# Performance work log

Hardware: AMD Instinct MI355X
Metric: run time of the kernel (lower is better)

Reference implementation:

```python
import jax, jax.numpy as jnp
import numpy as np

N_OSC = 2  # n: oscillator group size (pairwise oscillators)


def group_norm(c, w, b, num_groups, eps=1e-5):
    # c: [B, C, N]; torch.nn.GroupNorm semantics over (group-channels, N)
    B, C, N = c.shape
    g = c.reshape(B, num_groups, C // num_groups, N)
    mu = g.mean(axis=(2, 3), keepdims=True)
    var = g.var(axis=(2, 3), keepdims=True)
    g = (g - mu) / jnp.sqrt(var + eps)
    return g.reshape(B, C, N) * w[None, :, None] + b[None, :, None]


def normalize(x, n=N_OSC, eps=1e-6):
    # project each size-n group of channels onto the unit sphere
    B, N, C = x.shape
    v = x.reshape(B, N, C // n, n)
    nrm = jnp.linalg.norm(v, axis=-1, keepdims=True)
    return (v / (nrm + eps)).reshape(B, N, C)


def setup_inputs():
    key = jax.random.key(0)
    ks = jax.random.split(key, 4)
    B, C, N = 2, 16, 8192
    x = jax.random.normal(ks[0], (B, C, N), jnp.float32)
    c = jax.random.normal(ks[1], (B, C, N), jnp.float32)
    sc = jax.random.uniform(ks[2], (1, N, N), jnp.float32)  # dense structural connectivity
    gn_w = jnp.ones((C,), jnp.float32)
    gn_b = jnp.zeros((C,), jnp.float32)
    # learned per-edge coupling weight; scaled ~1/N so coupling is O(1)
    conn_w = jax.random.normal(ks[3], (N, N), jnp.float32) * (1.0 / N)
    # OmegaLayer param: init_omg * (1/sqrt(2)) * ones((ch//2, 1))
    omg_param = jnp.full((C // 2, 1), 1.0 / np.sqrt(2), jnp.float32)
    gamma = jnp.ones((1,), jnp.float32)
    return {"x": x, "c": c, "sc": sc, "gn_w": gn_w, "gn_b": gn_b,
            "conn_w": conn_w, "omg_param": omg_param, "gamma": gamma, "Q": 8}


def reference(x, c, sc, gn_w, gn_b, conn_w, omg_param, gamma, Q):
    n = N_OSC
    C = x.shape[1]
    # c_norm (GroupNorm with ch//n groups) then transpose [B,C,N] -> [B,N,C]
    y = group_norm(c, gn_w, gn_b, C // n)
    y = jnp.swapaxes(y, 1, 2)  # [B,N,C]
    xt = jnp.swapaxes(x, 1, 2)  # [B,N,C]
    A = sc[0] * conn_w  # weighted adjacency [N,N]
    omg = jnp.abs(omg_param)[None, None, :, 0]  # [1,1,C//2]; norm over last dim == abs
    g = gamma.reshape(())
    xt = normalize(xt)
    B, N, _ = xt.shape

    def step(xk, _):
        coup = jnp.einsum('mn,bnc->bmc', A, xk)  # graph coupling
        yt = coup + y
        xv = xk.reshape(B, N, C // n, n)
        yv = yt.reshape(B, N, C // n, n)
        sim = jnp.sum(xv * yv, axis=-1, keepdims=True)  # <x, y> per group
        y_proj = (yv - sim * xv).reshape(B, N, C)  # tangent projection
        xp = xk.reshape(B, N, C // 2, 2)
        omg_x = jnp.stack([omg * xp[..., 1], -omg * xp[..., 0]], axis=-1).reshape(B, N, C)
        xn = normalize(xk + g * (omg_x + y_proj))
        return xn, xn

    _, xs = jax.lax.scan(step, xt, None, length=Q)
    return xs  # [Q, B, N, C] (stacked list of per-step states)
```

## Files before the change

### kernel.cpp

```cpp
#include <hip/hip_runtime.h>
#include <hip/hip_bf16.h>

#define NB 2
#define NC 16
#define NN 8192
#define NBC 32
#define KS 16
#define SROWS 16
#define SWAVES 8
#define STEP_ELEMS (NB * NN * NC)

typedef float f32x4 __attribute__((ext_vector_type(4)));
typedef __bf16 bf16x8 __attribute__((ext_vector_type(8)));

__global__ void gn_stats_k(const float* __restrict__ c, float* __restrict__ stats) {
    int bg = blockIdx.x;
    const float* p = c + (size_t)bg * 16384;
    float s = 0.f, ss = 0.f;
    for (int i = threadIdx.x; i < 4096; i += 256) {
        float4 v = ((const float4*)p)[i];
        s  += v.x + v.y + v.z + v.w;
        ss += v.x*v.x + v.y*v.y + v.z*v.z + v.w*v.w;
    }
    #pragma unroll
    for (int o = 32; o; o >>= 1) { s += __shfl_down(s, o); ss += __shfl_down(ss, o); }
    __shared__ float sh[8];
    int w = threadIdx.x >> 6;
    if ((threadIdx.x & 63) == 0) { sh[w] = s; sh[w + 4] = ss; }
    __syncthreads();
    if (threadIdx.x == 0) {
        float S = sh[0]+sh[1]+sh[2]+sh[3], SS = sh[4]+sh[5]+sh[6]+sh[7];
        float mu = S * (1.f/16384.f);
        float var = SS * (1.f/16384.f) - mu*mu;
        stats[bg*2]   = mu;
        stats[bg*2+1] = rsqrtf(var + 1e-5f);
    }
}

__global__ void prep_xy_k(const float* __restrict__ x, const float* __restrict__ c,
                          const float* __restrict__ gnw, const float* __restrict__ gnb,
                          const float* __restrict__ stats,
                          float* __restrict__ y_arr, float* __restrict__ x0f,
                          __bf16* __restrict__ Xbf) {
    int tid = blockIdx.x * 256 + threadIdx.x;
    int n = tid & (NN - 1);
    int j = (tid >> 13) & 7;
    int b = tid >> 16;
    int ch0 = 2 * j;
    size_t r0 = ((size_t)(b * NC + ch0)) * NN + n;
    float c0 = c[r0], c1 = c[r0 + NN];
    float x0 = x[r0], x1 = x[r0 + NN];
    float mu = stats[(b*8 + j)*2], rstd = stats[(b*8 + j)*2 + 1];
    float y0 = (c0 - mu) * rstd * gnw[ch0]   + gnb[ch0];
    float y1 = (c1 - mu) * rstd * gnw[ch0+1] + gnb[ch0+1];
    int base = n * NBC + b * NC + ch0;
    y_arr[base] = y0; y_arr[base + 1] = y1;
    float inv = 1.f / (sqrtf(x0*x0 + x1*x1) + 1e-6f);
    x0 *= inv; x1 *= inv;
    size_t xi = ((size_t)(b * NN + n)) * NC + ch0;
    x0f[xi] = x0; x0f[xi + 1] = x1;
    Xbf[(size_t)(b*NC + ch0)     * NN + n] = (__bf16)x0;
    Xbf[(size_t)(b*NC + ch0 + 1) * NN + n] = (__bf16)x1;
}

__device__ inline bf16x8 cvt8(f32x4 s0, f32x4 s1, f32x4 w0, f32x4 w1) {
    bf16x8 r;
    r[0]=(__bf16)(s0[0]*w0[0]); r[1]=(__bf16)(s0[1]*w0[1]);
    r[2]=(__bf16)(s0[2]*w0[2]); r[3]=(__bf16)(s0[3]*w0[3]);
    r[4]=(__bf16)(s1[0]*w1[0]); r[5]=(__bf16)(s1[1]*w1[1]);
    r[6]=(__bf16)(s1[2]*w1[2]); r[7]=(__bf16)(s1[3]*w1[3]);
    return r;
}

__global__ __launch_bounds__(256) void prep_A_frag_k(const float* __restrict__ sc,
                                                     const float* __restrict__ cw,
                                                     __bf16* __restrict__ Af) {
    __shared__ __align__(16) __bf16 tb[16][520];
    int t = threadIdx.x;
    int p  = blockIdx.x >> 4;
    int kc = blockIdx.x & 15;
    #pragma unroll
    for (int it = 0; it < 4; ++it) {
        int e = it * 2048 + t * 8;
        int row = e >> 9;
        int kloc = e & 511;
        size_t src = (size_t)(p * 16 + row) * NN + kc * 512 + kloc;
        f32x4 s0 = ((const f32x4*)(sc + src))[0], s1 = ((const f32x4*)(sc + src))[1];
        f32x4 w0 = ((const f32x4*)(cw + src))[0], w1 = ((const f32x4*)(cw + src))[1];
        bf16x8 o = cvt8(s0, s1, w0, w1);
        int k32 = kloc >> 5;
        int lane_f = row + (((kloc & 31) >> 3) << 4);
        *(bf16x8*)(&tb[k32][lane_f * 8]) = o;
    }
    __syncthreads();
    size_t obase = ((size_t)p * 256 + kc * 16) * 512;
    #pragma unroll
    for (int it = 0; it < 4; ++it) {
        int f = it * 256 + t;
        int k32 = f >> 6;
        int lf  = f & 63;
        bf16x8 v = *(const bf16x8*)(&tb[k32][lf * 8]);
        *(bf16x8*)(Af + obase + (size_t)f * 8) = v;
    }
}

__global__ __launch_bounds__(512, 4) void gemm_frag_k(
    const __bf16* __restrict__ Af, const __bf16* __restrict__ Xc,
    float* __restrict__ coup)
{
    __shared__ float red[SWAVES][SROWS][36];
    int tid = threadIdx.x;
    int lane = tid & 63, w = tid >> 6;
    int mb = blockIdx.x;

    const __bf16* ap = Af + ((size_t)mb * 256 + w * 32) * 512 + lane * 8;
    int fr = lane & 15;
    int kg = (lane >> 4) * 8;
    const __bf16* xb0 = Xc + (size_t)fr * NN + w * 1024 + kg;
    const __bf16* xb1 = xb0 + (size_t)16 * NN;

    f32x4 acc0 = {0.f,0.f,0.f,0.f}, acc1 = {0.f,0.f,0.f,0.f};

    bf16x8 a0  = *(const bf16x8*)(ap);
    bf16x8 a1  = *(const bf16x8*)(ap + 512);
    bf16x8 b00 = *(const bf16x8*)(xb0);
    bf16x8 b01 = *(const bf16x8*)(xb0 + 32);
    bf16x8 b10 = *(const bf16x8*)(xb1);
    bf16x8 b11 = *(const bf16x8*)(xb1 + 32);
    #pragma unroll
    for (int it = 0; it < 15; ++it) {
        bf16x8 na0  = *(const bf16x8*)(ap  + (2 * it + 2) * 512);
        bf16x8 na1  = *(const bf16x8*)(ap  + (2 * it + 3) * 512);
        bf16x8 nb00 = *(const bf16x8*)(xb0 + it * 64 + 64);
        bf16x8 nb01 = *(const bf16x8*)(xb0 + it * 64 + 96);
        bf16x8 nb10 = *(const bf16x8*)(xb1 + it * 64 + 64);
        bf16x8 nb11 = *(const bf16x8*)(xb1 + it * 64 + 96);
        acc0 = __builtin_amdgcn_mfma_f32_16x16x32_bf16(a0, b00, acc0, 0, 0, 0);
        acc1 = __builtin_amdgcn_mfma_f32_16x16x32_bf16(a0, b10, acc1, 0, 0, 0);
        acc0 = __builtin_amdgcn_mfma_f32_16x16x32_bf16(a1, b01, acc0, 0, 0, 0);
        acc1 = __builtin_amdgcn_mfma_f32_16x16x32_bf16(a1, b11, acc1, 0, 0, 0);
        a0 = na0; a1 = na1; b00 = nb00; b01 = nb01; b10 = nb10; b11 = nb11;
    }
    acc0 = __builtin_amdgcn_mfma_f32_16x16x32_bf16(a0, b00, acc0, 0, 0, 0);
    acc1 = __builtin_amdgcn_mfma_f32_16x16x32_bf16(a0, b10, acc1, 0, 0, 0);
    acc0 = __builtin_amdgcn_mfma_f32_16x16x32_bf16(a1, b01, acc0, 0, 0, 0);
    acc1 = __builtin_amdgcn_mfma_f32_16x16x32_bf16(a1, b11, acc1, 0, 0, 0);

    int orow = (lane >> 4) * 4, ocol = lane & 15;
    #pragma unroll
    for (int r4 = 0; r4 < 4; ++r4) {
        red[w][orow + r4][ocol]      = acc0[r4];
        red[w][orow + r4][ocol + 16] = acc1[r4];
    }
    __syncthreads();

    if (tid < SROWS * 16) {
        int ch2 = tid & 15;
        int r_  = tid >> 4;
        float c0 = 0.f, c1 = 0.f;
        #pragma unroll
        for (int ww = 0; ww < SWAVES; ++ww) {
            c0 += red[ww][r_][2 * ch2];
            c1 += red[ww][r_][2 * ch2 + 1];
        }
        int n_ = mb * SROWS + r_;
        coup[(size_t)n_ * NBC + 2 * ch2]     = c0;
        coup[(size_t)n_ * NBC + 2 * ch2 + 1] = c1;
    }
}

__global__ void update_coup_k(const float* __restrict__ coup, const float* __restrict__ y_arr,
                              const float* __restrict__ omg, const float* __restrict__ gamma,
                              float* __restrict__ x0f, __bf16* __restrict__ Xbf,
                              float* __restrict__ out_k) {
    int tid = blockIdx.x * 256 + threadIdx.x;
    int pi = tid & 15;
    int b = pi >> 3, j = pi & 7;
    int n = tid >> 4;
    int base = n * NBC + b * NC + 2 * j;
    float c0 = coup[base];
    float c1 = coup[base + 1];
    float y0 = y_arr[base] + c0;
    float y1 = y_arr[base + 1] + c1;
    size_t xi = ((size_t)(b * NN + n)) * NC + 2 * j;
    float x0 = x0f[xi], x1 = x0f[xi + 1];
    float sim = x0 * y0 + x1 * y1;
    float p0 = y0 - sim * x0;
    float p1 = y1 - sim * x1;
    float om = fabsf(omg[j]);
    float g  = gamma[0];
    float v0 = x0 + g * ( om * x1 + p0);
    float v1 = x1 + g * (-om * x0 + p1);
    float inv = 1.f / (sqrtf(v0*v0 + v1*v1) + 1e-6f);
    v0 *= inv; v1 *= inv;
    out_k[xi] = v0; out_k[xi + 1] = v1;
    x0f[xi] = v0; x0f[xi + 1] = v1;
    Xbf[(size_t)(b*NC + 2*j)     * NN + n] = (__bf16)v0;
    Xbf[(size_t)(b*NC + 2*j + 1) * NN + n] = (__bf16)v1;
}

__device__ inline bf16x8 mulcvt8(const float* __restrict__ s, const float* __restrict__ w) {
    f32x4 s0 = ((const f32x4*)s)[0], s1 = ((const f32x4*)s)[1];
    f32x4 w0 = ((const f32x4*)w)[0], w1 = ((const f32x4*)w)[1];
    return cvt8(s0, s1, w0, w1);
}

__global__ __launch_bounds__(256) void gemm_step_fused_k(const float* __restrict__ sc,
                                                         const float* __restrict__ cw,
                                                         const __bf16* __restrict__ Xbf,
                                                         float* __restrict__ part) {
    int mb = blockIdx.x;
    int ks = blockIdx.y;
    int lane = threadIdx.x & 63;
    int w = threadIdx.x >> 6;
    int row = mb * 64 + w * 16 + (lane & 15);
    int kb  = (lane >> 4) * 8;
    int k0  = ks * (NN / KS);
    const int KC = NN / KS;
    f32x4 acc0 = {0.f,0.f,0.f,0.f}, acc1 = {0.f,0.f,0.f,0.f};
    const __bf16* bp0 = Xbf + (size_t)(lane & 15) * NN + k0 + kb;
    const __bf16* bp1 = bp0 + (size_t)16 * NN;
    const float* as = sc + (size_t)row * NN + k0 + kb;
    const float* aw = cw + (size_t)row * NN + k0 + kb;
    #pragma unroll 4
    for (int k = 0; k < KC; k += 32) {
        bf16x8 a  = mulcvt8(as + k, aw + k);
        bf16x8 b0 = *(const bf16x8*)(bp0 + k);
        bf16x8 b1 = *(const bf16x8*)(bp1 + k);
        acc0 = __builtin_amdgcn_mfma_f32_16x16x32_bf16(a, b0, acc0, 0, 0, 0);
        acc1 = __builtin_amdgcn_mfma_f32_16x16x32_bf16(a, b1, acc1, 0, 0, 0);
    }
    int orow = mb * 64 + w * 16 + (lane >> 4) * 4;
    int ocol = lane & 15;
    float* pp = part + (size_t)ks * NN * NBC + (size_t)orow * NBC + ocol;
    #pragma unroll
    for (int r = 0; r < 4; ++r) {
        pp[(size_t)r * NBC]      = acc0[r];
        pp[(size_t)r * NBC + 16] = acc1[r];
    }
}

__global__ void update_step_k(const float* __restrict__ part, const float* __restrict__ y_arr,
                              const float* __restrict__ omg, const float* __restrict__ gamma,
                              float* __restrict__ x0f, __bf16* __restrict__ Xbf,
                              float* __restrict__ out_k) {
    int tid = blockIdx.x * 256 + threadIdx.x;
    int pi = tid & 15;
    int b = pi >> 3, j = pi & 7;
    int n = tid >> 4;
    int base = n * NBC + b * NC + 2 * j;
    float c0 = 0.f, c1 = 0.f;
    #pragma unroll
    for (int ks = 0; ks < KS; ++ks) {
        const float* p = part + (size_t)ks * NN * NBC + base;
        c0 += p[0]; c1 += p[1];
    }
    float y0 = y_arr[base] + c0;
    float y1 = y_arr[base + 1] + c1;
    size_t xi = ((size_t)(b * NN + n)) * NC + 2 * j;
    float x0 = x0f[xi], x1 = x0f[xi + 1];
    float sim = x0 * y0 + x1 * y1;
    float p0 = y0 - sim * x0;
    float p1 = y1 - sim * x1;
    float om = fabsf(omg[j]);
    float g  = gamma[0];
    float v0 = x0 + g * ( om * x1 + p0);
    float v1 = x1 + g * (-om * x0 + p1);
    float inv = 1.f / (sqrtf(v0*v0 + v1*v1) + 1e-6f);
    v0 *= inv; v1 *= inv;
    out_k[xi] = v0; out_k[xi + 1] = v1;
    x0f[xi] = v0; x0f[xi + 1] = v1;
    Xbf[(size_t)(b*NC + 2*j)     * NN + n] = (__bf16)v0;
    Xbf[(size_t)(b*NC + 2*j + 1) * NN + n] = (__bf16)v1;
}

extern "C" void kernel_launch(void* const* d_in, const int* in_sizes, int n_in,
                              void* d_out, int out_size, void* d_ws, size_t ws_size,
                              hipStream_t stream) {
    const float* x     = (const float*)d_in[0];
    const float* c     = (const float*)d_in[1];
    const float* sc    = (const float*)d_in[2];
    const float* gnw   = (const float*)d_in[3];
    const float* gnb   = (const float*)d_in[4];
    const float* cw    = (const float*)d_in[5];
    const float* omg   = (const float*)d_in[6];
    const float* gamma = (const float*)d_in[7];
    float* out = (float*)d_out;
    int Q = out_size / STEP_ELEMS;

    const size_t szA    = (size_t)NN * NN * 2;
    const size_t szX    = (size_t)NBC * NN * 2;
    const size_t szX0f  = (size_t)NB * NN * NC * 4;
    const size_t szY    = (size_t)NN * NBC * 4;
    const size_t szCoup = (size_t)NN * NBC * 4;
    const size_t szPart = (size_t)KS * NN * NBC * 4;
    const size_t rest = szX + szX0f + szY + szCoup + szPart + 256;
    bool bigws = ws_size >= szA + rest;

    char* p = (char*)d_ws;
    __bf16* Af = nullptr;
    if (bigws) { Af = (__bf16*)p; p += szA; }
    __bf16* Xbf  = (__bf16*)p; p += szX;
    float* x0f   = (float*)p;  p += szX0f;
    float* y_arr = (float*)p;  p += szY;
    float* coup  = (float*)p;  p += szCoup;
    float* part  = (float*)p;  p += szPart;
    float* stats = (float*)p;  p += 256;

    gn_stats_k<<<16, 256, 0, stream>>>(c, stats);
    prep_xy_k<<<(NB * NN * 8) / 256, 256, 0, stream>>>(x, c, gnw, gnb, stats, y_arr, x0f, Xbf);

    if (bigws) {
        prep_A_frag_k<<<(NN / 16) * (NN / 512), 256, 0, stream>>>(sc, cw, Af);
        for (int q = 0; q < Q; ++q) {
            gemm_frag_k<<<NN / SROWS, SWAVES * 64, 0, stream>>>(Af, Xbf, coup);
            update_coup_k<<<(NB * NN * 8) / 256, 256, 0, stream>>>(
                coup, y_arr, omg, gamma, x0f, Xbf, out + (size_t)q * STEP_ELEMS);
        }
    } else {
        dim3 gg(NN / 64, KS);
        for (int q = 0; q < Q; ++q) {
            gemm_step_fused_k<<<gg, 256, 0, stream>>>(sc, cw, Xbf, part);
            update_step_k<<<(NB * NN * 8) / 256, 256, 0, stream>>>(
                part, y_arr, omg, gamma, x0f, Xbf, out + (size_t)q * STEP_ELEMS);
        }
    }
}
```

Before: 459.8 us.

## Process two row-blocks per GEMM workgroup with 16 waves and pad prep LDS

The per-step GEMM workgroup now computes 32 output rows instead of 16. It uses 16 waves, each covering a 512-wide K slice, so every loaded X fragment feeds MFMAs for two A row-blocks. This halves the grid and aims to cut redundant X loads from memory. The A-fragment prep kernel changes its LDS tile layout to a padded [16][4][17][8] shape, presumably to avoid bank conflicts, and issues its loads two at a time. The 1024-thread blocks with a larger reduction buffer may lower occupancy and lengthen the cross-wave reduction.

```diff
diff --git a/kernel.cpp b/kernel.cpp
--- a/kernel.cpp
+++ b/kernel.cpp
@@ -6,8 +6,6 @@
 #define NN 8192
 #define NBC 32
 #define KS 16
-#define SROWS 16
-#define SWAVES 8
 #define STEP_ELEMS (NB * NN * NC)
 
 typedef float f32x4 __attribute__((ext_vector_type(4)));
@@ -72,25 +70,30 @@
     return r;
 }
 
-__global__ __launch_bounds__(256) void prep_A_frag_k(const float* __restrict__ sc,
-                                                     const float* __restrict__ cw,
-                                                     __bf16* __restrict__ Af) {
-    __shared__ __align__(16) __bf16 tb[16][520];
+__global__ __launch_bounds__(256, 6) void prep_A_frag_k(const float* __restrict__ sc,
+                                                        const float* __restrict__ cw,
+                                                        __bf16* __restrict__ Af) {
+    __shared__ __align__(16) __bf16 tb[16][4][17][8];
     int t = threadIdx.x;
     int p  = blockIdx.x >> 4;
     int kc = blockIdx.x & 15;
     #pragma unroll
-    for (int it = 0; it < 4; ++it) {
-        int e = it * 2048 + t * 8;
-        int row = e >> 9;
-        int kloc = e & 511;
-        size_t src = (size_t)(p * 16 + row) * NN + kc * 512 + kloc;
-        f32x4 s0 = ((const f32x4*)(sc + src))[0], s1 = ((const f32x4*)(sc + src))[1];
-        f32x4 w0 = ((const f32x4*)(cw + src))[0], w1 = ((const f32x4*)(cw + src))[1];
-        bf16x8 o = cvt8(s0, s1, w0, w1);
-        int k32 = kloc >> 5;
-        int lane_f = row + (((kloc & 31) >> 3) << 4);
-        *(bf16x8*)(&tb[k32][lane_f * 8]) = o;
+    for (int h = 0; h < 2; ++h) {
+        f32x4 s[4], wv[4];
+        int e0 = (2*h) * 2048 + t * 8;
+        int e1 = (2*h + 1) * 2048 + t * 8;
+        size_t src0 = (size_t)(p * 16 + (e0 >> 9)) * NN + kc * 512 + (e0 & 511);
+        size_t src1 = (size_t)(p * 16 + (e1 >> 9)) * NN + kc * 512 + (e1 & 511);
+        s[0] = ((const f32x4*)(sc + src0))[0]; s[1] = ((const f32x4*)(sc + src0))[1];
+        s[2] = ((const f32x4*)(sc + src1))[0]; s[3] = ((const f32x4*)(sc + src1))[1];
+        wv[0] = ((const f32x4*)(cw + src0))[0]; wv[1] = ((const f32x4*)(cw + src0))[1];
+        wv[2] = ((const f32x4*)(cw + src1))[0]; wv[3] = ((const f32x4*)(cw + src1))[1];
+        bf16x8 o0 = cvt8(s[0], s[1], wv[0], wv[1]);
+        bf16x8 o1 = cvt8(s[2], s[3], wv[2], wv[3]);
+        int k0 = (e0 & 511) >> 5, oc0 = ((e0 & 31) >> 3), r0 = e0 >> 9;
+        int k1 = (e1 & 511) >> 5, oc1 = ((e1 & 31) >> 3), r1 = e1 >> 9;
+        *(bf16x8*)(&tb[k0][oc0][r0][0]) = o0;
+        *(bf16x8*)(&tb[k1][oc1][r1][0]) = o1;
     }
     __syncthreads();
     size_t obase = ((size_t)p * 256 + kc * 16) * 512;
@@ -99,71 +102,88 @@
         int f = it * 256 + t;
         int k32 = f >> 6;
         int lf  = f & 63;
-        bf16x8 v = *(const bf16x8*)(&tb[k32][lf * 8]);
+        bf16x8 v = *(const bf16x8*)(&tb[k32][lf >> 4][lf & 15][0]);
         *(bf16x8*)(Af + obase + (size_t)f * 8) = v;
     }
 }
 
-__global__ __launch_bounds__(512, 4) void gemm_frag_k(
+__global__ __launch_bounds__(1024, 4) void gemm_frag_k(
     const __bf16* __restrict__ Af, const __bf16* __restrict__ Xc,
     float* __restrict__ coup)
 {
-    __shared__ float red[SWAVES][SROWS][36];
+    __shared__ float red[16][32][36];
     int tid = threadIdx.x;
     int lane = tid & 63, w = tid >> 6;
     int mb = blockIdx.x;
 
-    const __bf16* ap = Af + ((size_t)mb * 256 + w * 32) * 512 + lane * 8;
+    const __bf16* ap0 = Af + ((size_t)(2 * mb)     * 256 + w * 16) * 512 + lane * 8;
+    const __bf16* ap1 = Af + ((size_t)(2 * mb + 1) * 256 + w * 16) * 512 + lane * 8;
     int fr = lane & 15;
     int kg = (lane >> 4) * 8;
-    const __bf16* xb0 = Xc + (size_t)fr * NN + w * 1024 + kg;
+    const __bf16* xb0 = Xc + (size_t)fr * NN + w * 512 + kg;
     const __bf16* xb1 = xb0 + (size_t)16 * NN;
 
-    f32x4 acc0 = {0.f,0.f,0.f,0.f}, acc1 = {0.f,0.f,0.f,0.f};
-
-    bf16x8 a0  = *(const bf16x8*)(ap);
-    bf16x8 a1  = *(const bf16x8*)(ap + 512);
+    f32x4 acc00 = {0.f,0.f,0.f,0.f}, acc01 = {0.f,0.f,0.f,0.f};
+    f32x4 acc10 = {0.f,0.f,0.f,0.f}, acc11 = {0.f,0.f,0.f,0.f};
+
+    bf16x8 a00 = *(const bf16x8*)(ap0);
+    bf16x8 a01 = *(const bf16x8*)(ap0 + 512);
+    bf16x8 a10 = *(const bf16x8*)(ap1);
+    bf16x8 a11 = *(const bf16x8*)(ap1 + 512);
     bf16x8 b00 = *(const bf16x8*)(xb0);
     bf16x8 b01 = *(const bf16x8*)(xb0 + 32);
     bf16x8 b10 = *(const bf16x8*)(xb1);
     bf16x8 b11 = *(const bf16x8*)(xb1 + 32);
     #pragma unroll
-    for (int it = 0; it < 15; ++it) {
-        bf16x8 na0  = *(const bf16x8*)(ap  + (2 * it + 2) * 512);
-        bf16x8 na1  = *(const bf16x8*)(ap  + (2 * it + 3) * 512);
+    for (int it = 0; it < 7; ++it) {
+        bf16x8 na00 = *(const bf16x8*)(ap0 + (2 * it + 2) * 512);
+        bf16x8 na01 = *(const bf16x8*)(ap0 + (2 * it + 3) * 512);
+        bf16x8 na10 = *(const bf16x8*)(ap1 + (2 * it + 2) * 512);
+        bf16x8 na11 = *(const bf16x8*)(ap1 + (2 * it + 3) * 512);
         bf16x8 nb00 = *(const bf16x8*)(xb0 + it * 64 + 64);
         bf16x8 nb01 = *(const bf16x8*)(xb0 + it * 64 + 96);
         bf16x8 nb10 = *(const bf16x8*)(xb1 + it * 64 + 64);
         bf16x8 nb11 = *(const bf16x8*)(xb1 + it * 64 + 96);
-        acc0 = __builtin_amdgcn_mfma_f32_16x16x32_bf16(a0, b00, acc0, 0, 0, 0);
-        acc1 = __builtin_amdgcn_mfma_f32_16x16x32_bf16(a0, b10, acc1, 0, 0, 0);
-        acc0 = __builtin_amdgcn_mfma_f32_16x16x32_bf16(a1, b01, acc0, 0, 0, 0);
-        acc1 = __builtin_amdgcn_mfma_f32_16x16x32_bf16(a1, b11, acc1, 0, 0, 0);
-        a0 = na0; a1 = na1; b00 = nb00; b01 = nb01; b10 = nb10; b11 = nb11;
-    }
-    acc0 = __builtin_amdgcn_mfma_f32_16x16x32_bf16(a0, b00, acc0, 0, 0, 0);
-    acc1 = __builtin_amdgcn_mfma_f32_16x16x32_bf16(a0, b10, acc1, 0, 0, 0);
-    acc0 = __builtin_amdgcn_mfma_f32_16x16x32_bf16(a1, b01, acc0, 0, 0, 0);
-    acc1 = __builtin_amdgcn_mfma_f32_16x16x32_bf16(a1, b11, acc1, 0, 0, 0);
+        acc00 = __builtin_amdgcn_mfma_f32_16x16x32_bf16(a00, b00, acc00, 0, 0, 0);
+        acc01 = __builtin_amdgcn_mfma_f32_16x16x32_bf16(a00, b10, acc01, 0, 0, 0);
+        acc10 = __builtin_amdgcn_mfma_f32_16x16x32_bf16(a10, b00, acc10, 0, 0, 0);
+        acc11 = __builtin_amdgcn_mfma_f32_16x16x32_bf16(a10, b10, acc11, 0, 0, 0);
+        acc00 = __builtin_amdgcn_mfma_f32_16x16x32_bf16(a01, b01, acc00, 0, 0, 0);
+        acc01 = __builtin_amdgcn_mfma_f32_16x16x32_bf16(a01, b11, acc01, 0, 0, 0);
+        acc10 = __builtin_amdgcn_mfma_f32_16x16x32_bf16(a11, b01, acc10, 0, 0, 0);
+        acc11 = __builtin_amdgcn_mfma_f32_16x16x32_bf16(a11, b11, acc11, 0, 0, 0);
+        a00 = na00; a01 = na01; a10 = na10; a11 = na11;
+        b00 = nb00; b01 = nb01; b10 = nb10; b11 = nb11;
+    }
+    acc00 = __builtin_amdgcn_mfma_f32_16x16x32_bf16(a00, b00, acc00, 0, 0, 0);
+    acc01 = __builtin_amdgcn_mfma_f32_16x16x32_bf16(a00, b10, acc01, 0, 0, 0);
+    acc10 = __builtin_amdgcn_mfma_f32_16x16x32_bf16(a10, b00, acc10, 0, 0, 0);
+    acc11 = __builtin_amdgcn_mfma_f32_16x16x32_bf16(a10, b10, acc11, 0, 0, 0);
+    acc00 = __builtin_amdgcn_mfma_f32_16x16x32_bf16(a01, b01, acc00, 0, 0, 0);
+    acc01 = __builtin_amdgcn_mfma_f32_16x16x32_bf16(a01, b11, acc01, 0, 0, 0);
+    acc10 = __builtin_amdgcn_mfma_f32_16x16x32_bf16(a11, b01, acc10, 0, 0, 0);
+    acc11 = __builtin_amdgcn_mfma_f32_16x16x32_bf16(a11, b11, acc11, 0, 0, 0);
 
     int orow = (lane >> 4) * 4, ocol = lane & 15;
     #pragma unroll
     for (int r4 = 0; r4 < 4; ++r4) {
-        red[w][orow + r4][ocol]      = acc0[r4];
-        red[w][orow + r4][ocol + 16] = acc1[r4];
+        red[w][orow + r4][ocol]           = acc00[r4];
+        red[w][orow + r4][ocol + 16]      = acc01[r4];
+        red[w][16 + orow + r4][ocol]      = acc10[r4];
+        red[w][16 + orow + r4][ocol + 16] = acc11[r4];
     }
     __syncthreads();
 
-    if (tid < SROWS * 16) {
+    if (tid < 32 * 16) {
         int ch2 = tid & 15;
         int r_  = tid >> 4;
         float c0 = 0.f, c1 = 0.f;
         #pragma unroll
-        for (int ww = 0; ww < SWAVES; ++ww) {
+        for (int ww = 0; ww < 16; ++ww) {
             c0 += red[ww][r_][2 * ch2];
             c1 += red[ww][r_][2 * ch2 + 1];
         }
-        int n_ = mb * SROWS + r_;
+        int n_ = mb * 32 + r_;
         coup[(size_t)n_ * NBC + 2 * ch2]     = c0;
         coup[(size_t)n_ * NBC + 2 * ch2 + 1] = c1;
     }
@@ -313,7 +333,7 @@
     if (bigws) {
         prep_A_frag_k<<<(NN / 16) * (NN / 512), 256, 0, stream>>>(sc, cw, Af);
         for (int q = 0; q < Q; ++q) {
-            gemm_frag_k<<<NN / SROWS, SWAVES * 64, 0, stream>>>(Af, Xbf, coup);
+            gemm_frag_k<<<NN / 32, 1024, 0, stream>>>(Af, Xbf, coup);
             update_coup_k<<<(NB * NN * 8) / 256, 256, 0, stream>>>(
                 coup, y_arr, omg, gamma, x0f, Xbf, out + (size_t)q * STEP_ELEMS);
         }
```

Measured after the change: 397.0 us. 1.16x faster.
